# Performance work log

Hardware: AMD Instinct MI355X
Metric: run time of the kernel (lower is better)

Reference implementation:

```python
import jax, jax.numpy as jnp
import numpy as np

B, L, H = 8192, 64, 128
DEPTH = 3
EPS = 1e-5


def setup_inputs() -> dict:
    key = jax.random.key(0)
    ks = jax.random.split(key, 1 + 6)
    hidden_states = jax.random.normal(ks[0], (B, L, H), dtype=jnp.float32)
    # stacked per-layer params: Linear(H,H) -> LayerNorm(H) -> ReLU -> Linear(H, H//2)
    s1 = 1.0 / np.sqrt(H)
    W1 = jax.random.uniform(ks[1], (DEPTH, H, H), jnp.float32, -s1, s1)
    b1 = jax.random.uniform(ks[2], (DEPTH, H), jnp.float32, -s1, s1)
    gamma = jnp.ones((DEPTH, H), jnp.float32)
    beta = jnp.zeros((DEPTH, H), jnp.float32)
    W2 = jax.random.uniform(ks[3], (DEPTH, H, H // 2), jnp.float32, -s1, s1)
    b2 = jax.random.uniform(ks[4], (DEPTH, H // 2), jnp.float32, -s1, s1)
    return {
        "hidden_states": hidden_states,
        "W1": W1, "b1": b1, "gamma": gamma, "beta": beta,
        "W2": W2, "b2": b2,
        "lengths": L,
    }


def _layernorm(x, g, b):
    mu = jnp.mean(x, axis=-1, keepdims=True)
    var = jnp.mean(jnp.square(x - mu), axis=-1, keepdims=True)
    return (x - mu) * jax.lax.rsqrt(var + EPS) * g + b


def reference(hidden_states, W1, b1, gamma, beta, W2, b2, lengths):
    # hidden_states: [B, L, H]; max(lengths) == L
    x = hidden_states
    for i in range(DEPTH):
        h = jnp.einsum('blh,hk->blk', x, W1[i]) + b1[i]          # [B, L, H]
        h = jax.nn.relu(_layernorm(h, gamma[i], beta[i]))
        x1 = jnp.einsum('blh,hk->blk', h, W2[i]) + b2[i]          # [B, L, H//2]
        x2 = jnp.max(x1, axis=1, keepdims=True)                   # max-pool over seq
        x2 = jnp.broadcast_to(x2, x1.shape)                       # repeat to L
        x = jnp.concatenate([x1, x2], axis=2)                     # [B, L, H]
    return jnp.max(x, axis=1)                                     # [B, H]
```

## Files before the change

### kernel.cpp

```cpp
#include <hip/hip_runtime.h>

#define NB 8192
#define NL 64
#define NH 128

typedef __bf16 bf16x8 __attribute__((ext_vector_type(8)));
typedef float f32x4 __attribute__((ext_vector_type(4)));
typedef float f32x2 __attribute__((ext_vector_type(2)));
typedef unsigned short ushort8 __attribute__((ext_vector_type(8)));

__device__ __host__ __forceinline__ int p2l(int p) {
  return (p & ~31) + ((p & 1) << 4) + ((p & 31) >> 1);
}
__device__ __host__ __forceinline__ int pi2(int p) {
  return (p & 1) ? 64 + (p >> 1) : (p >> 1);
}

__device__ __forceinline__ unsigned pk2(float lo, float hi) {
  union { __bf16 b[2]; unsigned u; } t;
  t.b[0] = (__bf16)lo; t.b[1] = (__bf16)hi;
  return t.u;
}

__global__ __launch_bounds__(256) void repack_w(const float* __restrict__ W1,
                                                const float* __restrict__ W2,
                                                const float* __restrict__ gamma,
                                                const float* __restrict__ beta,
                                                unsigned short* __restrict__ wp1,
                                                unsigned short* __restrict__ wp2,
                                                float* __restrict__ gbt) {
  int t = blockIdx.x * 256 + threadIdx.x;
  int lane = t & 63, g = t >> 6;
  if (g < 96) {
    int layer = g >> 5, rem = g & 31, nt = rem >> 2, ks = rem & 3;
    int n = nt * 16 + (lane & 15);
    int kb = ks * 32 + (lane >> 4) * 8;
    ushort8 v;
#pragma unroll
    for (int r = 0; r < 8; ++r) {
      int k = kb + r;
      int srck = (layer == 0) ? k : pi2(k);
      union { __bf16 b; unsigned short u; } c;
      c.b = (__bf16)W1[(layer * 128 + srck) * 128 + n];
      v[r] = c.u;
    }
    *reinterpret_cast<ushort8*>(wp1 + ((size_t)g * 64 + lane) * 8) = v;
  } else if (g < 144) {
    int g2 = g - 96;
    int layer = g2 >> 4, rem = g2 & 15, nt = rem >> 2, ks = rem & 3;
    int n = nt * 16 + (lane & 15);
    int kb = ks * 32 + (lane >> 4) * 8;
    ushort8 v;
#pragma unroll
    for (int r = 0; r < 8; ++r) {
      union { __bf16 b; unsigned short u; } c;
      c.b = (__bf16)W2[(layer * 128 + p2l(kb + r)) * 64 + n];
      v[r] = c.u;
    }
    *reinterpret_cast<ushort8*>(wp2 + ((size_t)g2 * 64 + lane) * 8) = v;
  } else if (g < 150) {
    int g2 = g - 144;
    int layer = g2 >> 1, param = g2 & 1;
    const float* src = (param == 0 ? gamma : beta) + layer * 128;
    float* dst = gbt + layer * 288 + param * 144;
    int p0 = lane * 2;
#pragma unroll
    for (int u = 0; u < 2; ++u) {
      int p = p0 + u;
      dst[(p >> 5) * 36 + (p & 31)] = src[p2l(p)];
    }
  }
}

__global__ __launch_bounds__(256) void fused_mlp(
    const float* __restrict__ hidden,
    const float* __restrict__ b1,
    const float* __restrict__ b2,
    const unsigned short* __restrict__ wp1u,
    const unsigned short* __restrict__ wp2u,
    const float* __restrict__ gbt,
    float* __restrict__ out) {
  __shared__ __align__(16) unsigned short xAu[NL * NH];
  __shared__ __align__(16) unsigned short xBu[NL * NH];
  __shared__ __align__(16) float gbuf[864];

  const int tid = threadIdx.x;
  const int wave = tid >> 6, lane = tid & 63;
  const int ci = lane & 15, lg = lane >> 4;
  char* xA = reinterpret_cast<char*>(xAu);
  char* xB = reinterpret_cast<char*>(xBu);

  const int abase = ci * 256;
  const int axor = ci << 4;

  if (tid < 96) {
#pragma unroll
    for (int u = 0; u < 9; ++u) gbuf[tid * 9 + u] = gbt[tid * 9 + u];
  }

  const float* src = hidden + (size_t)blockIdx.x * (NL * NH);
#pragma unroll
  for (int i = 0; i < 4; ++i) {
    int f = i * 256 + tid;
    int row = f >> 4;
    int cb = (f & 15) * 16;
    const float4* p = reinterpret_cast<const float4*>(src + f * 8);
    float4 a = p[0], bq = p[1];
    bf16x8 v;
    v[0] = (__bf16)a.x;  v[1] = (__bf16)a.y;  v[2] = (__bf16)a.z;  v[3] = (__bf16)a.w;
    v[4] = (__bf16)bq.x; v[5] = (__bf16)bq.y; v[6] = (__bf16)bq.z; v[7] = (__bf16)bq.w;
    *reinterpret_cast<bf16x8*>(xA + row * 256 + (cb ^ ((row & 15) << 4))) = v;
  }
  __syncthreads();

  for (int layer = 0; layer < 3; ++layer) {
    const unsigned short* wl1 = wp1u + (size_t)layer * 16384;
    const float bv0 = b1[layer * 128 + wave * 32 + ci];
    const float bv1 = b1[layer * 128 + wave * 32 + 16 + ci];
    const int dby = (wave * 16 + ci) * 4;

    f32x4 acc[4][2];
#pragma unroll
    for (int mt = 0; mt < 4; ++mt) {
      acc[mt][0] = f32x4{bv0, bv0, bv0, bv0};
      acc[mt][1] = f32x4{bv1, bv1, bv1, bv1};
    }
#pragma unroll
    for (int ks = 0; ks < 4; ++ks) {
      bf16x8 bf0 = *reinterpret_cast<const bf16x8*>(
          wl1 + (((wave * 2 + 0) * 4 + ks) * 64 + lane) * 8);
      bf16x8 bf1 = *reinterpret_cast<const bf16x8*>(
          wl1 + (((wave * 2 + 1) * 4 + ks) * 64 + lane) * 8);
      int cbx = ((ks * 64 + lg * 16) ^ axor) + abase;
#pragma unroll
      for (int mt = 0; mt < 4; ++mt) {
        bf16x8 af = *reinterpret_cast<const bf16x8*>(xA + mt * 4096 + cbx);
        acc[mt][0] = __builtin_amdgcn_mfma_f32_16x16x32_bf16(af, bf0, acc[mt][0], 0, 0, 0);
        acc[mt][1] = __builtin_amdgcn_mfma_f32_16x16x32_bf16(af, bf1, acc[mt][1], 0, 0, 0);
      }
    }
#pragma unroll
    for (int mt = 0; mt < 4; ++mt)
#pragma unroll
      for (int r = 0; r < 4; ++r) {
        int row = mt * 16 + lg * 4 + r;
        *reinterpret_cast<unsigned*>(
            xB + row * 256 + (dby ^ ((lg * 4 + r) << 4))) =
            pk2(acc[mt][0][r], acc[mt][1][r]);
      }
    __syncthreads();

    const unsigned short* wl2 = wp2u + (size_t)layer * 8192;
    bf16x8 w2f[4];
#pragma unroll
    for (int ks = 0; ks < 4; ++ks)
      w2f[ks] = *reinterpret_cast<const bf16x8*>(
          wl2 + ((wave * 4 + ks) * 64 + lane) * 8);
    float b2v = b2[layer * 64 + wave * 16 + ci];

    {
      const int row = wave * 16 + (lane >> 2);
      const int q = lane & 3;
      const int rb = row * 256, rx = (lane >> 2) << 4;
      bf16x8 h0 = *reinterpret_cast<const bf16x8*>(xB + rb + ((q * 64 + 0) ^ rx));
      bf16x8 h1 = *reinterpret_cast<const bf16x8*>(xB + rb + ((q * 64 + 16) ^ rx));
      bf16x8 h2 = *reinterpret_cast<const bf16x8*>(xB + rb + ((q * 64 + 32) ^ rx));
      bf16x8 h3 = *reinterpret_cast<const bf16x8*>(xB + rb + ((q * 64 + 48) ^ rx));
      f32x2 f[16];
#pragma unroll
      for (int cch = 0; cch < 4; ++cch) {
        bf16x8 hv = (cch == 0) ? h0 : (cch == 1) ? h1 : (cch == 2) ? h2 : h3;
#pragma unroll
        for (int j2 = 0; j2 < 4; ++j2)
          f[cch * 4 + j2] = f32x2{(float)hv[j2 * 2], (float)hv[j2 * 2 + 1]};
      }
      f32x2 s2 = {0.f, 0.f}, q2 = {0.f, 0.f};
#pragma unroll
      for (int i = 0; i < 16; ++i) { s2 += f[i]; q2 += f[i] * f[i]; }
      float s = s2.x + s2.y, sq = q2.x + q2.y;
      s += __shfl_xor(s, 1);  sq += __shfl_xor(sq, 1);
      s += __shfl_xor(s, 2);  sq += __shfl_xor(sq, 2);
      float mu = s * (1.f / 128.f);
      float var = sq * (1.f / 128.f) - mu * mu;
      float rs = rsqrtf(var + 1e-5f);
      const f32x2* gl = reinterpret_cast<const f32x2*>(gbuf + layer * 288 + q * 36);
      const f32x2* bl = reinterpret_cast<const f32x2*>(gbuf + layer * 288 + 144 + q * 36);
#pragma unroll
      for (int cch = 0; cch < 4; ++cch) {
        union { unsigned u[4]; bf16x8 v; } yy;
#pragma unroll
        for (int j2 = 0; j2 < 4; ++j2) {
          int i = cch * 4 + j2;
          f32x2 a2 = gl[i] * rs;
          f32x2 c2 = bl[i] - a2 * mu;
          f32x2 y2 = f[i] * a2 + c2;
          yy.u[j2] = pk2(fmaxf(y2.x, 0.f), fmaxf(y2.y, 0.f));
        }
        *reinterpret_cast<bf16x8*>(xB + rb + ((q * 64 + cch * 16) ^ rx)) = yy.v;
      }
    }
    __syncthreads();

    f32x4 acc2[4];
#pragma unroll
    for (int mt = 0; mt < 4; ++mt) acc2[mt] = f32x4{b2v, b2v, b2v, b2v};
#pragma unroll
    for (int ks = 0; ks < 4; ++ks) {
      int cbx = ((ks * 64 + lg * 16) ^ axor) + abase;
#pragma unroll
      for (int mt = 0; mt < 4; ++mt) {
        bf16x8 af = *reinterpret_cast<const bf16x8*>(xB + mt * 4096 + cbx);
        acc2[mt] = __builtin_amdgcn_mfma_f32_16x16x32_bf16(af, w2f[ks], acc2[mt], 0, 0, 0);
      }
    }

    float mm;
    {
      float m = -3.0e38f;
#pragma unroll
      for (int mt = 0; mt < 4; ++mt)
#pragma unroll
        for (int r = 0; r < 4; ++r) m = fmaxf(m, acc2[mt][r]);
      m = fmaxf(m, __shfl_xor(m, 16));
      m = fmaxf(m, __shfl_xor(m, 32));
      mm = m;
    }

    if (layer < 2) {
#pragma unroll
      for (int mt = 0; mt < 4; ++mt)
#pragma unroll
        for (int r = 0; r < 4; ++r) {
          int row = mt * 16 + lg * 4 + r;
          *reinterpret_cast<unsigned*>(
              xA + row * 256 + (dby ^ ((lg * 4 + r) << 4))) =
              pk2(acc2[mt][r], mm);
        }
      __syncthreads();
    } else {
      if (lg == 0) {
        size_t o = (size_t)blockIdx.x * 128 + wave * 16 + ci;
        out[o] = mm;
        out[o + 64] = mm;
      }
    }
  }
}

extern "C" void kernel_launch(void* const* d_in, const int* in_sizes, int n_in,
                              void* d_out, int out_size, void* d_ws, size_t ws_size,
                              hipStream_t stream) {
  const float* hidden = (const float*)d_in[0];
  const float* W1 = (const float*)d_in[1];
  const float* b1 = (const float*)d_in[2];
  const float* gamma = (const float*)d_in[3];
  const float* beta = (const float*)d_in[4];
  const float* W2 = (const float*)d_in[5];
  const float* b2 = (const float*)d_in[6];
  (void)in_sizes; (void)n_in; (void)out_size; (void)ws_size;

  unsigned short* wp1 = (unsigned short*)d_ws;
  unsigned short* wp2 = wp1 + 3 * 8 * 4 * 64 * 8;
  float* gbt = (float*)(wp2 + 3 * 4 * 4 * 64 * 8);
  float* out = (float*)d_out;

  repack_w<<<38, 256, 0, stream>>>(W1, W2, gamma, beta, wp1, wp2, gbt);
  fused_mlp<<<NB, 256, 0, stream>>>(hidden, b1, b2, wp1, wp2, gbt, out);
}
```

Before: 142.0 us.

## Swap MFMA operand order so outputs are transposed, enabling 16-byte LDS stores

Both GEMMs now pass the weights as the A operand and the activations as the B operand, so each lane's accumulator holds four consecutive output features for one sequence row instead of four rows for one feature. The intermediate bf16 results can then be written to shared memory as one 16-byte vector store per tile rather than four 4-byte scattered stores. Bias loads and the final output store become vectorized. The max-pool reduction grows to a four-step shuffle over 16 lanes on four values. Layer-1 weight fragments are preloaded into registers and layer-2 weights are loaded later, which raises register pressure.

Measured after the change: 157.3 us. 10.8% more time.

```diff
diff --git a/kernel.cpp b/kernel.cpp
--- a/kernel.cpp
+++ b/kernel.cpp
@@ -7,6 +7,7 @@
 typedef __bf16 bf16x8 __attribute__((ext_vector_type(8)));
 typedef float f32x4 __attribute__((ext_vector_type(4)));
 typedef float f32x2 __attribute__((ext_vector_type(2)));
+typedef unsigned uint4v __attribute__((ext_vector_type(4)));
 typedef unsigned short ushort8 __attribute__((ext_vector_type(8)));
 
 __device__ __host__ __forceinline__ int p2l(int p) {
@@ -92,6 +93,7 @@
 
   const int abase = ci * 256;
   const int axor = ci << 4;
+  const int wbase = ci * 256 + ((wave * 64 + lg * 16) ^ axor);
 
   if (tid < 96) {
 #pragma unroll
@@ -115,48 +117,36 @@
 
   for (int layer = 0; layer < 3; ++layer) {
     const unsigned short* wl1 = wp1u + (size_t)layer * 16384;
-    const float bv0 = b1[layer * 128 + wave * 32 + ci];
-    const float bv1 = b1[layer * 128 + wave * 32 + 16 + ci];
-    const int dby = (wave * 16 + ci) * 4;
-
+    bf16x8 w1f[2][4];
+#pragma unroll
+    for (int nt2 = 0; nt2 < 2; ++nt2)
+#pragma unroll
+      for (int ks = 0; ks < 4; ++ks)
+        w1f[nt2][ks] = *reinterpret_cast<const bf16x8*>(
+            wl1 + (((wave * 2 + nt2) * 4 + ks) * 64 + lane) * 8);
+    f32x4 bA = *reinterpret_cast<const f32x4*>(b1 + layer * 128 + wave * 32 + lg * 4);
+    f32x4 bB = *reinterpret_cast<const f32x4*>(b1 + layer * 128 + wave * 32 + 16 + lg * 4);
     f32x4 acc[4][2];
 #pragma unroll
+    for (int mt = 0; mt < 4; ++mt) { acc[mt][0] = bA; acc[mt][1] = bB; }
+#pragma unroll
+    for (int ks = 0; ks < 4; ++ks) {
+      int cbx = ((ks * 64 + lg * 16) ^ axor) + abase;
+#pragma unroll
+      for (int mt = 0; mt < 4; ++mt) {
+        bf16x8 xf = *reinterpret_cast<const bf16x8*>(xA + mt * 4096 + cbx);
+        acc[mt][0] = __builtin_amdgcn_mfma_f32_16x16x32_bf16(w1f[0][ks], xf, acc[mt][0], 0, 0, 0);
+        acc[mt][1] = __builtin_amdgcn_mfma_f32_16x16x32_bf16(w1f[1][ks], xf, acc[mt][1], 0, 0, 0);
+      }
+    }
+#pragma unroll
     for (int mt = 0; mt < 4; ++mt) {
-      acc[mt][0] = f32x4{bv0, bv0, bv0, bv0};
-      acc[mt][1] = f32x4{bv1, bv1, bv1, bv1};
-    }
-#pragma unroll
-    for (int ks = 0; ks < 4; ++ks) {
-      bf16x8 bf0 = *reinterpret_cast<const bf16x8*>(
-          wl1 + (((wave * 2 + 0) * 4 + ks) * 64 + lane) * 8);
-      bf16x8 bf1 = *reinterpret_cast<const bf16x8*>(
-          wl1 + (((wave * 2 + 1) * 4 + ks) * 64 + lane) * 8);
-      int cbx = ((ks * 64 + lg * 16) ^ axor) + abase;
-#pragma unroll
-      for (int mt = 0; mt < 4; ++mt) {
-        bf16x8 af = *reinterpret_cast<const bf16x8*>(xA + mt * 4096 + cbx);
-        acc[mt][0] = __builtin_amdgcn_mfma_f32_16x16x32_bf16(af, bf0, acc[mt][0], 0, 0, 0);
-        acc[mt][1] = __builtin_amdgcn_mfma_f32_16x16x32_bf16(af, bf1, acc[mt][1], 0, 0, 0);
-      }
-    }
-#pragma unroll
-    for (int mt = 0; mt < 4; ++mt)
-#pragma unroll
-      for (int r = 0; r < 4; ++r) {
-        int row = mt * 16 + lg * 4 + r;
-        *reinterpret_cast<unsigned*>(
-            xB + row * 256 + (dby ^ ((lg * 4 + r) << 4))) =
-            pk2(acc[mt][0][r], acc[mt][1][r]);
-      }
+      uint4v w;
+#pragma unroll
+      for (int r = 0; r < 4; ++r) w[r] = pk2(acc[mt][0][r], acc[mt][1][r]);
+      *reinterpret_cast<uint4v*>(xB + mt * 4096 + wbase) = w;
+    }
     __syncthreads();
-
-    const unsigned short* wl2 = wp2u + (size_t)layer * 8192;
-    bf16x8 w2f[4];
-#pragma unroll
-    for (int ks = 0; ks < 4; ++ks)
-      w2f[ks] = *reinterpret_cast<const bf16x8*>(
-          wl2 + ((wave * 4 + ks) * 64 + lane) * 8);
-    float b2v = b2[layer * 64 + wave * 16 + ci];
 
     {
       const int row = wave * 16 + (lane >> 2);
@@ -201,47 +191,49 @@
     }
     __syncthreads();
 
+    const unsigned short* wl2 = wp2u + (size_t)layer * 8192;
+    bf16x8 w2f[4];
+#pragma unroll
+    for (int ks = 0; ks < 4; ++ks)
+      w2f[ks] = *reinterpret_cast<const bf16x8*>(
+          wl2 + ((wave * 4 + ks) * 64 + lane) * 8);
+    f32x4 b2v = *reinterpret_cast<const f32x4*>(b2 + layer * 64 + wave * 16 + lg * 4);
     f32x4 acc2[4];
 #pragma unroll
-    for (int mt = 0; mt < 4; ++mt) acc2[mt] = f32x4{b2v, b2v, b2v, b2v};
+    for (int mt = 0; mt < 4; ++mt) acc2[mt] = b2v;
 #pragma unroll
     for (int ks = 0; ks < 4; ++ks) {
       int cbx = ((ks * 64 + lg * 16) ^ axor) + abase;
 #pragma unroll
       for (int mt = 0; mt < 4; ++mt) {
-        bf16x8 af = *reinterpret_cast<const bf16x8*>(xB + mt * 4096 + cbx);
-        acc2[mt] = __builtin_amdgcn_mfma_f32_16x16x32_bf16(af, w2f[ks], acc2[mt], 0, 0, 0);
-      }
-    }
-
-    float mm;
-    {
-      float m = -3.0e38f;
-#pragma unroll
-      for (int mt = 0; mt < 4; ++mt)
-#pragma unroll
-        for (int r = 0; r < 4; ++r) m = fmaxf(m, acc2[mt][r]);
-      m = fmaxf(m, __shfl_xor(m, 16));
-      m = fmaxf(m, __shfl_xor(m, 32));
-      mm = m;
-    }
+        bf16x8 xf = *reinterpret_cast<const bf16x8*>(xB + mt * 4096 + cbx);
+        acc2[mt] = __builtin_amdgcn_mfma_f32_16x16x32_bf16(w2f[ks], xf, acc2[mt], 0, 0, 0);
+      }
+    }
+
+    f32x4 mm;
+#pragma unroll
+    for (int r = 0; r < 4; ++r)
+      mm[r] = fmaxf(fmaxf(acc2[0][r], acc2[1][r]), fmaxf(acc2[2][r], acc2[3][r]));
+#pragma unroll
+    for (int o = 1; o < 16; o <<= 1)
+#pragma unroll
+      for (int r = 0; r < 4; ++r) mm[r] = fmaxf(mm[r], __shfl_xor(mm[r], o));
 
     if (layer < 2) {
 #pragma unroll
-      for (int mt = 0; mt < 4; ++mt)
-#pragma unroll
-        for (int r = 0; r < 4; ++r) {
-          int row = mt * 16 + lg * 4 + r;
-          *reinterpret_cast<unsigned*>(
-              xA + row * 256 + (dby ^ ((lg * 4 + r) << 4))) =
-              pk2(acc2[mt][r], mm);
-        }
+      for (int mt = 0; mt < 4; ++mt) {
+        uint4v w;
+#pragma unroll
+        for (int r = 0; r < 4; ++r) w[r] = pk2(acc2[mt][r], mm[r]);
+        *reinterpret_cast<uint4v*>(xA + mt * 4096 + wbase) = w;
+      }
       __syncthreads();
     } else {
-      if (lg == 0) {
-        size_t o = (size_t)blockIdx.x * 128 + wave * 16 + ci;
-        out[o] = mm;
-        out[o + 64] = mm;
+      if (ci == 0) {
+        float* o = out + (size_t)blockIdx.x * 128 + wave * 16 + lg * 4;
+        *reinterpret_cast<f32x4*>(o) = mm;
+        *reinterpret_cast<f32x4*>(o + 64) = mm;
       }
     }
   }
```
